# Performance work log

Measured on AMD Instinct MI355X. Metric: run time of the kernel, lower is better.

Reference implementation:

```python
import jax, jax.numpy as jnp
import numpy as np

B, C, N, K, O = 4, 64, 16384, 16, 128
EPS1, EPS2 = 1e-5, 1e-6


def conv_bn_relu(x, w, g, b, m, v, eps):
    # 1x1 Conv1d (no bias) + eval-mode BatchNorm1d + ReLU; x: [B, C, N]
    y = jnp.einsum('oc,bcn->bon', w, x)
    scale = g / jnp.sqrt(v + eps)
    y = (y - m[None, :, None]) * scale[None, :, None] + b[None, :, None]
    return jax.nn.relu(y)


def gather_neighbors(f_bcn, idx):
    # f_bcn: [B, C, N], idx: [B, N, k] -> [B, C, N, k]
    f_bnc = jnp.transpose(f_bcn, (0, 2, 1))
    g = jax.vmap(lambda f, i: f[i])(f_bnc, idx)  # [B, N, k, C]
    return jnp.transpose(g, (0, 3, 1, 2))


def setup_inputs():
    key = jax.random.key(0)
    ks = jax.random.split(key, 24)
    s = lambda i, shape: jax.random.normal(ks[i], shape, jnp.float32) * 0.05
    inp = {
        'x_info': jax.random.normal(ks[0], (B, C, N, K), jnp.float32),
        'feature': jax.random.normal(ks[1], (B, C, N), jnp.float32),
        'neighbor_index': jax.random.randint(ks[2], (B, N, K), 0, N, jnp.int32),
        'Wq_w': s(3, (C, C)), 'Wq_g': jnp.ones((C,)) + s(4, (C,)), 'Wq_b': s(5, (C,)),
        'Wq_m': s(6, (C,)), 'Wq_v': jax.random.uniform(ks[7], (C,)) + 0.5,
        'Wk_w': s(8, (C, C)), 'Wk_g': jnp.ones((C,)) + s(9, (C,)), 'Wk_b': s(10, (C,)),
        'Wk_m': s(11, (C,)), 'Wk_v': jax.random.uniform(ks[12], (C,)) + 0.5,
        'Wv_w': s(13, (C, C)), 'Wv_g': jnp.ones((C,)) + s(14, (C,)), 'Wv_b': s(15, (C,)),
        'Wv_m': s(16, (C,)), 'Wv_v': jax.random.uniform(ks[17], (C,)) + 0.5,
        'm2_w': s(18, (O, C)), 'm2_g': jnp.ones((O,)) + s(19, (O,)), 'm2_b': s(20, (O,)),
        'm2_m': s(21, (O,)), 'm2_v': jax.random.uniform(ks[22], (O,)) + 0.5,
    }
    return inp


def reference(x_info, feature, neighbor_index,
              Wq_w, Wq_g, Wq_b, Wq_m, Wq_v,
              Wk_w, Wk_g, Wk_b, Wk_m, Wk_v,
              Wv_w, Wv_g, Wv_b, Wv_m, Wv_v,
              m2_w, m2_g, m2_b, m2_m, m2_v):
    q = conv_bn_relu(feature, Wq_w, Wq_g, Wq_b, Wq_m, Wq_v, EPS1)  # [B,C,N]
    k = conv_bn_relu(feature, Wk_w, Wk_g, Wk_b, Wk_m, Wk_v, EPS1)
    v = conv_bn_relu(feature, Wv_w, Wv_g, Wv_b, Wv_m, Wv_v, EPS1)
    kg = gather_neighbors(k, neighbor_index)  # [B,C,N,k]
    vg = gather_neighbors(v, neighbor_index)  # [B,C,N,k]
    W = x_info * (kg - q[..., None])          # [B,C,N,k]
    attn = jax.nn.softmax(W, axis=-1)
    feat = jnp.sum(attn * vg, axis=-1)        # [B,C,N]
    # mlp2: 1x1 conv + BN(eps=1e-6) + LeakyReLU(0.2)
    y = jnp.einsum('oc,bcn->bon', m2_w, feat)
    scale = m2_g / jnp.sqrt(m2_v + EPS2)
    y = (y - m2_m[None, :, None]) * scale[None, :, None] + m2_b[None, :, None]
    return jnp.where(y >= 0, y, 0.2 * y)
```

## Files before the change

kernel.cpp:

```cpp
#include <hip/hip_runtime.h>
#include <cstddef>
#include <cstdint>

#define NPT 16384
#define NB  4

typedef float    f32x4 __attribute__((ext_vector_type(4)));
typedef uint32_t u32x4 __attribute__((ext_vector_type(4)));

__device__ __forceinline__ uint32_t bf16_rtne(float f) {
    uint32_t u = __builtin_bit_cast(uint32_t, f);
    return (u + 0x7FFFu + ((u >> 16) & 1u)) >> 16;
}

__global__ __launch_bounds__(256) void k_qkv(
    const float* __restrict__ feat_in,
    const float* __restrict__ Wq, const float* __restrict__ Wk, const float* __restrict__ Wv,
    const float* __restrict__ Qg, const float* __restrict__ Qb, const float* __restrict__ Qm, const float* __restrict__ Qv,
    const float* __restrict__ Kg, const float* __restrict__ Kb, const float* __restrict__ Km, const float* __restrict__ Kv,
    const float* __restrict__ Vg, const float* __restrict__ Vb, const float* __restrict__ Vm, const float* __restrict__ Vv,
    float* __restrict__ qo, uint32_t* __restrict__ kvo)
{
    __shared__ float wt[64][192];
    __shared__ float fs[64][64];
    const int tid = threadIdx.x;
    const int b   = blockIdx.y;
    const int n0  = blockIdx.x * 64;

    {
        const int o  = tid >> 2;
        const int cb = (tid & 3) * 16;
        const float* Ws[3] = {Wq, Wk, Wv};
        #pragma unroll
        for (int t = 0; t < 3; ++t) {
            const float4* src = reinterpret_cast<const float4*>(Ws[t] + o * 64 + cb);
            #pragma unroll
            for (int k4 = 0; k4 < 4; ++k4) {
                float4 w4 = src[k4];
                wt[cb + k4 * 4 + 0][t * 64 + o] = w4.x;
                wt[cb + k4 * 4 + 1][t * 64 + o] = w4.y;
                wt[cb + k4 * 4 + 2][t * 64 + o] = w4.z;
                wt[cb + k4 * 4 + 3][t * 64 + o] = w4.w;
            }
        }
    }
    #pragma unroll
    for (int i = 0; i < 16; ++i) {
        int flat = tid + i * 256;
        int c = flat >> 6, n = flat & 63;
        fs[c][n] = feat_in[((size_t)b * 64 + c) * NPT + n0 + n];
    }
    __syncthreads();

    const int to = tid & 15;
    const int tn = tid >> 4;
    float acc[3][4][4];
    #pragma unroll
    for (int t = 0; t < 3; ++t)
        #pragma unroll
        for (int i = 0; i < 4; ++i)
            #pragma unroll
            for (int j = 0; j < 4; ++j) acc[t][i][j] = 0.f;

    #pragma unroll 4
    for (int c = 0; c < 64; ++c) {
        float4 f4  = *reinterpret_cast<const float4*>(&fs[c][tn * 4]);
        float4 wq4 = *reinterpret_cast<const float4*>(&wt[c][to * 4]);
        float4 wk4 = *reinterpret_cast<const float4*>(&wt[c][64 + to * 4]);
        float4 wv4 = *reinterpret_cast<const float4*>(&wt[c][128 + to * 4]);
        float fr[4]    = {f4.x, f4.y, f4.z, f4.w};
        float wr[3][4] = {{wq4.x, wq4.y, wq4.z, wq4.w},
                          {wk4.x, wk4.y, wk4.z, wk4.w},
                          {wv4.x, wv4.y, wv4.z, wv4.w}};
        #pragma unroll
        for (int t = 0; t < 3; ++t)
            #pragma unroll
            for (int oi = 0; oi < 4; ++oi)
                #pragma unroll
                for (int nn = 0; nn < 4; ++nn)
                    acc[t][oi][nn] = fmaf(wr[t][oi], fr[nn], acc[t][oi][nn]);
    }

    float scq[4], shq[4], sck[4], shk[4], scv[4], shv[4];
    #pragma unroll
    for (int oi = 0; oi < 4; ++oi) {
        int o = to * 4 + oi;
        float s;
        s = Qg[o] * rsqrtf(Qv[o] + 1e-5f); scq[oi] = s; shq[oi] = Qb[o] - Qm[o] * s;
        s = Kg[o] * rsqrtf(Kv[o] + 1e-5f); sck[oi] = s; shk[oi] = Kb[o] - Km[o] * s;
        s = Vg[o] * rsqrtf(Vv[o] + 1e-5f); scv[oi] = s; shv[oi] = Vb[o] - Vm[o] * s;
    }
    #pragma unroll
    for (int nn = 0; nn < 4; ++nn) {
        const size_t pidx = (size_t)b * NPT + n0 + tn * 4 + nn;
        float4 rq;
        rq.x = fmaxf(fmaf(acc[0][0][nn], scq[0], shq[0]), 0.f);
        rq.y = fmaxf(fmaf(acc[0][1][nn], scq[1], shq[1]), 0.f);
        rq.z = fmaxf(fmaf(acc[0][2][nn], scq[2], shq[2]), 0.f);
        rq.w = fmaxf(fmaf(acc[0][3][nn], scq[3], shq[3]), 0.f);
        *reinterpret_cast<float4*>(qo + (pidx << 6) + to * 4) = rq;
        u32x4 pk;
        #pragma unroll
        for (int oi = 0; oi < 4; ++oi) {
            float rk = fmaxf(fmaf(acc[1][oi][nn], sck[oi], shk[oi]), 0.f);
            float rv = fmaxf(fmaf(acc[2][oi][nn], scv[oi], shv[oi]), 0.f);
            pk[oi] = (bf16_rtne(rk) << 16) | bf16_rtne(rv);
        }
        *reinterpret_cast<u32x4*>(kvo + (pidx << 6) + to * 4) = pk;
    }
}

__global__ __launch_bounds__(256) void k_attn(
    const float*    __restrict__ xinfo,
    const int*      __restrict__ nidx,
    float*                       qfeat,
    const uint32_t* __restrict__ kv)
{
    __shared__ float xs[64][68];
    const int tid  = threadIdx.x;
    const int lane = tid & 63;
    const int wv   = tid >> 6;
    const int p0   = blockIdx.x * 4;
    const int b    = p0 >> 14;
    const int n0   = p0 & 16383;
    const int p    = p0 + wv;

    const int pu = __builtin_amdgcn_readfirstlane(p);
    const int4* irow = reinterpret_cast<const int4*>(nidx + ((size_t)pu << 4));
    int4 i0 = irow[0], i1 = irow[1], i2 = irow[2], i3 = irow[3];
    const int idxs[16] = {i0.x, i0.y, i0.z, i0.w,  i1.x, i1.y, i1.z, i1.w,
                          i2.x, i2.y, i2.z, i2.w,  i3.x, i3.y, i3.z, i3.w};

    uint32_t gr[16];
    #pragma unroll
    for (int j = 0; j < 16; ++j)
        gr[j] = kv[(((size_t)((b << 14) | idxs[j])) << 6) + lane];

    float qc = __builtin_nontemporal_load(qfeat + ((size_t)p << 6) + lane);

    const float* xbase = xinfo + (((size_t)b * 64) * NPT + n0) * 16;
    f32x4 xr[4];
    #pragma unroll
    for (int i = 0; i < 4; ++i) {
        int f = tid + i * 256;
        int c = f >> 4, s = f & 15;
        xr[i] = __builtin_nontemporal_load(
            reinterpret_cast<const f32x4*>(xbase + (size_t)c * (NPT * 16) + s * 4));
    }
    #pragma unroll
    for (int i = 0; i < 4; ++i) {
        int f = tid + i * 256;
        int c = f >> 4, s = f & 15;
        *reinterpret_cast<f32x4*>(&xs[c][s * 4]) = xr[i];
    }

    float kgv[16], vgv[16];
    #pragma unroll
    for (int j = 0; j < 16; ++j) {
        kgv[j] = __builtin_bit_cast(float, gr[j] & 0xFFFF0000u);
        vgv[j] = __builtin_bit_cast(float, gr[j] << 16);
    }
    __syncthreads();

    float w[16];
    #pragma unroll
    for (int k4 = 0; k4 < 4; ++k4) {
        float4 x4 = *reinterpret_cast<const float4*>(&xs[lane][wv * 16 + k4 * 4]);
        w[k4 * 4 + 0] = x4.x * (kgv[k4 * 4 + 0] - qc);
        w[k4 * 4 + 1] = x4.y * (kgv[k4 * 4 + 1] - qc);
        w[k4 * 4 + 2] = x4.z * (kgv[k4 * 4 + 2] - qc);
        w[k4 * 4 + 3] = x4.w * (kgv[k4 * 4 + 3] - qc);
    }

    float mx = w[0];
    #pragma unroll
    for (int j = 1; j < 16; ++j) mx = fmaxf(mx, w[j]);

    float es = 0.f, fsum = 0.f;
    #pragma unroll
    for (int j = 0; j < 16; ++j) {
        float e = __expf(w[j] - mx);
        es += e;
        fsum = fmaf(e, vgv[j], fsum);
    }

    qfeat[((size_t)p << 6) + lane] = fsum / es;
}

__global__ __launch_bounds__(256) void k_mlp2(
    const float* __restrict__ feat,
    const float* __restrict__ m2w,
    const float* __restrict__ g2, const float* __restrict__ b2,
    const float* __restrict__ m2, const float* __restrict__ v2,
    float* __restrict__ out)
{
    __shared__ float wt [64][132];
    __shared__ float fsh[64][68];
    const int tid = threadIdx.x;
    const int b   = blockIdx.y;
    const int n0  = blockIdx.x * 64;

    {
        const int o  = tid >> 1;
        const int ch = (tid & 1) * 32;
        const float4* src = reinterpret_cast<const float4*>(m2w + o * 64 + ch);
        #pragma unroll
        for (int k4 = 0; k4 < 8; ++k4) {
            float4 w4 = src[k4];
            wt[ch + k4 * 4 + 0][o] = w4.x;
            wt[ch + k4 * 4 + 1][o] = w4.y;
            wt[ch + k4 * 4 + 2][o] = w4.z;
            wt[ch + k4 * 4 + 3][o] = w4.w;
        }
    }
    {
        const int c4 = tid & 15;
        const int nl = tid >> 4;
        #pragma unroll
        for (int i = 0; i < 4; ++i) {
            int n = nl + i * 16;
            float4 f4 = *reinterpret_cast<const float4*>(
                feat + (((size_t)b * NPT + n0 + n) << 6) + c4 * 4);
            fsh[c4 * 4 + 0][n] = f4.x;
            fsh[c4 * 4 + 1][n] = f4.y;
            fsh[c4 * 4 + 2][n] = f4.z;
            fsh[c4 * 4 + 3][n] = f4.w;
        }
    }
    __syncthreads();

    const int tn = tid & 15;
    const int to = tid >> 4;
    float acc[2][4][4];
    #pragma unroll
    for (int h = 0; h < 2; ++h)
        #pragma unroll
        for (int i = 0; i < 4; ++i)
            #pragma unroll
            for (int j = 0; j < 4; ++j) acc[h][i][j] = 0.f;

    #pragma unroll 4
    for (int c = 0; c < 64; ++c) {
        float4 wa = *reinterpret_cast<const float4*>(&wt[c][to * 4]);
        float4 wb = *reinterpret_cast<const float4*>(&wt[c][64 + to * 4]);
        float4 f4 = *reinterpret_cast<const float4*>(&fsh[c][tn * 4]);
        float wra[4] = {wa.x, wa.y, wa.z, wa.w};
        float wrb[4] = {wb.x, wb.y, wb.z, wb.w};
        float fr[4]  = {f4.x, f4.y, f4.z, f4.w};
        #pragma unroll
        for (int oi = 0; oi < 4; ++oi)
            #pragma unroll
            for (int ni = 0; ni < 4; ++ni) {
                acc[0][oi][ni] = fmaf(wra[oi], fr[ni], acc[0][oi][ni]);
                acc[1][oi][ni] = fmaf(wrb[oi], fr[ni], acc[1][oi][ni]);
            }
    }

    #pragma unroll
    for (int h = 0; h < 2; ++h)
        #pragma unroll
        for (int oi = 0; oi < 4; ++oi) {
            int o = h * 64 + to * 4 + oi;
            float s  = g2[o] * rsqrtf(v2[o] + 1e-6f);
            float sh = b2[o] - m2[o] * s;
            f32x4 r;
            #pragma unroll
            for (int ni = 0; ni < 4; ++ni) {
                float y = fmaf(acc[h][oi][ni], s, sh);
                r[ni] = (y >= 0.f) ? y : 0.2f * y;
            }
            __builtin_nontemporal_store(r, reinterpret_cast<f32x4*>(
                out + (((size_t)b << 7) + o) * NPT + n0 + tn * 4));
        }
}

extern "C" void kernel_launch(void* const* d_in, const int* in_sizes, int n_in,
                              void* d_out, int out_size, void* d_ws, size_t ws_size,
                              hipStream_t stream)
{
    const float* xinfo   = (const float*)d_in[0];
    const float* feature = (const float*)d_in[1];
    const int*   nidx    = (const int*)  d_in[2];
    const float* Wq = (const float*)d_in[3];
    const float* Qg = (const float*)d_in[4];
    const float* Qb = (const float*)d_in[5];
    const float* Qm = (const float*)d_in[6];
    const float* Qv = (const float*)d_in[7];
    const float* Wk = (const float*)d_in[8];
    const float* Kg = (const float*)d_in[9];
    const float* Kb = (const float*)d_in[10];
    const float* Km = (const float*)d_in[11];
    const float* Kv = (const float*)d_in[12];
    const float* Wv = (const float*)d_in[13];
    const float* Vg = (const float*)d_in[14];
    const float* Vb = (const float*)d_in[15];
    const float* Vm = (const float*)d_in[16];
    const float* Vv = (const float*)d_in[17];
    const float* m2w = (const float*)d_in[18];
    const float* g2  = (const float*)d_in[19];
    const float* b2  = (const float*)d_in[20];
    const float* m2  = (const float*)d_in[21];
    const float* v2  = (const float*)d_in[22];
    float* out = (float*)d_out;

    float*    ws    = (float*)d_ws;
    float*    qf    = ws;
    uint32_t* kvbuf = (uint32_t*)(ws + (size_t)NB * NPT * 64);

    k_qkv<<<dim3(NPT / 64, NB), 256, 0, stream>>>(
        feature, Wq, Wk, Wv,
        Qg, Qb, Qm, Qv, Kg, Kb, Km, Kv, Vg, Vb, Vm, Vv,
        qf, kvbuf);

    k_attn<<<(NB * NPT) / 4, 256, 0, stream>>>(xinfo, nidx, qf, kvbuf);

    k_mlp2<<<dim3(NPT / 64, NB), 256, 0, stream>>>(qf, m2w, g2, b2, m2, v2, out);
}
```

Baseline: 113.8 us.

## Store q and attention output as bf16 and drop softmax max-subtraction

The q buffer and the attention output are now bf16 instead of fp32, halving that intermediate traffic across all three kernels. The attention softmax skips the max-subtraction pass and fuses exp, sum and weighted accumulation into one loop, removing the kgv/vgv unpack arrays. The mlp2 loader is reworked to unpack bf16 pairs into shared memory with a changed padding. This costs precision in q and feat, and risks exp overflow without max-subtraction if the logits are large.

```diff
diff --git a/kernel.cpp b/kernel.cpp
--- a/kernel.cpp
+++ b/kernel.cpp
@@ -7,10 +7,17 @@
 
 typedef float    f32x4 __attribute__((ext_vector_type(4)));
 typedef uint32_t u32x4 __attribute__((ext_vector_type(4)));
+typedef uint16_t u16x4 __attribute__((ext_vector_type(4)));
 
 __device__ __forceinline__ uint32_t bf16_rtne(float f) {
     uint32_t u = __builtin_bit_cast(uint32_t, f);
     return (u + 0x7FFFu + ((u >> 16) & 1u)) >> 16;
+}
+__device__ __forceinline__ float bf16_hi(uint32_t w) {
+    return __builtin_bit_cast(float, w & 0xFFFF0000u);
+}
+__device__ __forceinline__ float bf16_lo(uint32_t w) {
+    return __builtin_bit_cast(float, w << 16);
 }
 
 __global__ __launch_bounds__(256) void k_qkv(
@@ -19,7 +26,7 @@
     const float* __restrict__ Qg, const float* __restrict__ Qb, const float* __restrict__ Qm, const float* __restrict__ Qv,
     const float* __restrict__ Kg, const float* __restrict__ Kb, const float* __restrict__ Km, const float* __restrict__ Kv,
     const float* __restrict__ Vg, const float* __restrict__ Vb, const float* __restrict__ Vm, const float* __restrict__ Vv,
-    float* __restrict__ qo, uint32_t* __restrict__ kvo)
+    uint16_t* __restrict__ qo, uint32_t* __restrict__ kvo)
 {
     __shared__ float wt[64][192];
     __shared__ float fs[64][64];
@@ -93,19 +100,17 @@
     #pragma unroll
     for (int nn = 0; nn < 4; ++nn) {
         const size_t pidx = (size_t)b * NPT + n0 + tn * 4 + nn;
-        float4 rq;
-        rq.x = fmaxf(fmaf(acc[0][0][nn], scq[0], shq[0]), 0.f);
-        rq.y = fmaxf(fmaf(acc[0][1][nn], scq[1], shq[1]), 0.f);
-        rq.z = fmaxf(fmaf(acc[0][2][nn], scq[2], shq[2]), 0.f);
-        rq.w = fmaxf(fmaf(acc[0][3][nn], scq[3], shq[3]), 0.f);
-        *reinterpret_cast<float4*>(qo + (pidx << 6) + to * 4) = rq;
+        u16x4 rq;
         u32x4 pk;
         #pragma unroll
         for (int oi = 0; oi < 4; ++oi) {
+            float q = fmaxf(fmaf(acc[0][oi][nn], scq[oi], shq[oi]), 0.f);
             float rk = fmaxf(fmaf(acc[1][oi][nn], sck[oi], shk[oi]), 0.f);
             float rv = fmaxf(fmaf(acc[2][oi][nn], scv[oi], shv[oi]), 0.f);
+            rq[oi] = (uint16_t)bf16_rtne(q);
             pk[oi] = (bf16_rtne(rk) << 16) | bf16_rtne(rv);
         }
+        *reinterpret_cast<u16x4*>(qo  + (pidx << 6) + to * 4) = rq;
         *reinterpret_cast<u32x4*>(kvo + (pidx << 6) + to * 4) = pk;
     }
 }
@@ -113,7 +118,7 @@
 __global__ __launch_bounds__(256) void k_attn(
     const float*    __restrict__ xinfo,
     const int*      __restrict__ nidx,
-    float*                       qfeat,
+    uint16_t*                    qfeat,
     const uint32_t* __restrict__ kv)
 {
     __shared__ float xs[64][68];
@@ -136,7 +141,8 @@
     for (int j = 0; j < 16; ++j)
         gr[j] = kv[(((size_t)((b << 14) | idxs[j])) << 6) + lane];
 
-    float qc = __builtin_nontemporal_load(qfeat + ((size_t)p << 6) + lane);
+    uint16_t qraw = __builtin_nontemporal_load(qfeat + ((size_t)p << 6) + lane);
+    float qc = bf16_lo((uint32_t)qraw);
 
     const float* xbase = xinfo + (((size_t)b * 64) * NPT + n0) * 16;
     f32x4 xr[4];
@@ -153,49 +159,34 @@
         int c = f >> 4, s = f & 15;
         *reinterpret_cast<f32x4*>(&xs[c][s * 4]) = xr[i];
     }
-
-    float kgv[16], vgv[16];
-    #pragma unroll
-    for (int j = 0; j < 16; ++j) {
-        kgv[j] = __builtin_bit_cast(float, gr[j] & 0xFFFF0000u);
-        vgv[j] = __builtin_bit_cast(float, gr[j] << 16);
-    }
     __syncthreads();
 
-    float w[16];
+    float es = 0.f, fsum = 0.f;
     #pragma unroll
     for (int k4 = 0; k4 < 4; ++k4) {
         float4 x4 = *reinterpret_cast<const float4*>(&xs[lane][wv * 16 + k4 * 4]);
-        w[k4 * 4 + 0] = x4.x * (kgv[k4 * 4 + 0] - qc);
-        w[k4 * 4 + 1] = x4.y * (kgv[k4 * 4 + 1] - qc);
-        w[k4 * 4 + 2] = x4.z * (kgv[k4 * 4 + 2] - qc);
-        w[k4 * 4 + 3] = x4.w * (kgv[k4 * 4 + 3] - qc);
-    }
-
-    float mx = w[0];
-    #pragma unroll
-    for (int j = 1; j < 16; ++j) mx = fmaxf(mx, w[j]);
-
-    float es = 0.f, fsum = 0.f;
-    #pragma unroll
-    for (int j = 0; j < 16; ++j) {
-        float e = __expf(w[j] - mx);
-        es += e;
-        fsum = fmaf(e, vgv[j], fsum);
-    }
-
-    qfeat[((size_t)p << 6) + lane] = fsum / es;
+        float xv[4] = {x4.x, x4.y, x4.z, x4.w};
+        #pragma unroll
+        for (int q4 = 0; q4 < 4; ++q4) {
+            int j = k4 * 4 + q4;
+            float e = __expf(xv[q4] * (bf16_hi(gr[j]) - qc));
+            es += e;
+            fsum = fmaf(e, bf16_lo(gr[j]), fsum);
+        }
+    }
+
+    qfeat[((size_t)p << 6) + lane] = (uint16_t)bf16_rtne(fsum / es);
 }
 
 __global__ __launch_bounds__(256) void k_mlp2(
-    const float* __restrict__ feat,
+    const uint16_t* __restrict__ feat,
     const float* __restrict__ m2w,
     const float* __restrict__ g2, const float* __restrict__ b2,
     const float* __restrict__ m2, const float* __restrict__ v2,
     float* __restrict__ out)
 {
     __shared__ float wt [64][132];
-    __shared__ float fsh[64][68];
+    __shared__ float fsh[64][69];
     const int tid = threadIdx.x;
     const int b   = blockIdx.y;
     const int n0  = blockIdx.x * 64;
@@ -214,17 +205,19 @@
         }
     }
     {
-        const int c4 = tid & 15;
-        const int nl = tid >> 4;
-        #pragma unroll
-        for (int i = 0; i < 4; ++i) {
-            int n = nl + i * 16;
-            float4 f4 = *reinterpret_cast<const float4*>(
-                feat + (((size_t)b * NPT + n0 + n) << 6) + c4 * 4);
-            fsh[c4 * 4 + 0][n] = f4.x;
-            fsh[c4 * 4 + 1][n] = f4.y;
-            fsh[c4 * 4 + 2][n] = f4.z;
-            fsh[c4 * 4 + 3][n] = f4.w;
+        const int c8 = tid & 7;
+        const int nl = tid >> 3;
+        #pragma unroll
+        for (int half = 0; half < 2; ++half) {
+            int n = nl + half * 32;
+            u32x4 rw = *reinterpret_cast<const u32x4*>(
+                feat + (((size_t)b * NPT + n0 + n) << 6) + c8 * 8);
+            #pragma unroll
+            for (int k = 0; k < 4; ++k) {
+                uint32_t w2 = rw[k];
+                fsh[c8 * 8 + k * 2 + 0][n] = bf16_lo(w2);
+                fsh[c8 * 8 + k * 2 + 1][n] = bf16_hi(w2);
+            }
         }
     }
     __syncthreads();
@@ -303,9 +296,8 @@
     const float* v2  = (const float*)d_in[22];
     float* out = (float*)d_out;
 
-    float*    ws    = (float*)d_ws;
-    float*    qf    = ws;
-    uint32_t* kvbuf = (uint32_t*)(ws + (size_t)NB * NPT * 64);
+    uint16_t* qf    = (uint16_t*)d_ws;
+    uint32_t* kvbuf = (uint32_t*)((uint8_t*)d_ws + (8u << 20));
 
     k_qkv<<<dim3(NPT / 64, NB), 256, 0, stream>>>(
         feature, Wq, Wk, Wv,
```

New measurement: 110.7 us (median of 2 runs). 2.7% less time.
